# Optimization experiments

Hardware: AMD Instinct MI355X
Metric: run time of the kernel (lower is better)

The kernel has to match this reference:

```python
import jax, jax.numpy as jnp
import numpy as np

DIM = 1024
HEADS = 16
HEAD_DIM = DIM // HEADS
SCALE = HEAD_DIM ** -0.5
EPS = 1e-5


def _ln(x, g, b):
    m = jnp.mean(x, axis=-1, keepdims=True)
    v = jnp.mean((x - m) ** 2, axis=-1, keepdims=True)
    return (x - m) * jax.lax.rsqrt(v + EPS) * g + b


def setup_inputs() -> dict:
    key = jax.random.key(0)
    ks = jax.random.split(key, 12)
    B, N, C = 4, 1024, DIM
    s = lambda fan: 1.0 / np.sqrt(fan)
    return {
        "src_q": jax.random.normal(ks[0], (B, N, C), jnp.float32),
        "src_kv": jax.random.normal(ks[1], (B, N, C), jnp.float32),
        "gq": jnp.ones((C,), jnp.float32), "bq": jnp.zeros((C,), jnp.float32),
        "gkv": jnp.ones((C,), jnp.float32), "bkv": jnp.zeros((C,), jnp.float32),
        "Wq": jax.random.normal(ks[2], (C, C), jnp.float32) * s(C),
        "Wkv": jax.random.normal(ks[3], (C, 2 * C), jnp.float32) * s(C),
        "Wproj": jax.random.normal(ks[4], (C, C), jnp.float32) * s(C),
        "bproj": jnp.zeros((C,), jnp.float32),
        "gn": jnp.ones((C,), jnp.float32), "bn": jnp.zeros((C,), jnp.float32),
        "W1": jax.random.normal(ks[5], (C, 4 * C), jnp.float32) * s(C),
        "b1": jnp.zeros((4 * C,), jnp.float32),
        "W2": jax.random.normal(ks[6], (4 * C, C), jnp.float32) * s(4 * C),
        "b2": jnp.zeros((C,), jnp.float32),
    }


def reference(src_q, src_kv, gq, bq, gkv, bkv, Wq, Wkv, Wproj, bproj,
              gn, bn, W1, b1, W2, b2):
    B, N, C = src_q.shape
    qn = _ln(src_q, gq, bq)
    kvn = _ln(src_kv, gkv, bkv)
    # Q: [B, H, N, d]
    Q = (qn @ Wq).reshape(B, N, HEADS, HEAD_DIM).transpose(0, 2, 1, 3)
    KV = (kvn @ Wkv).reshape(B, N, 2, HEADS, HEAD_DIM).transpose(2, 0, 3, 1, 4)
    K, V = KV[0], KV[1]
    attn = jnp.einsum('bhqd,bhkd->bhqk', Q, K) * SCALE
    attn = jax.nn.softmax(attn, axis=-1)
    # NOTE: original code multiplies by scale a second time here (faithful)
    x = jnp.einsum('bhqk,bhkd->bhqd', attn, V) * SCALE
    x = x.transpose(0, 2, 1, 3).reshape(B, N, C)
    x = x @ Wproj + bproj
    src = src_q + x               # residual (drop_path = identity in eval)
    src = _ln(src, gn, bn)
    h = jax.nn.gelu(src @ W1 + b1, approximate=False)
    src2 = h @ W2 + b2
    return src + src2
```

## Files before the change

### kernel.cpp

```cpp
#include <hip/hip_runtime.h>
#include <hip/hip_bf16.h>
#include <math.h>

typedef __bf16 bf16;
typedef __bf16 bf16x2 __attribute__((ext_vector_type(2)));
typedef __bf16 bf16x8 __attribute__((ext_vector_type(8)));
typedef float f32x4 __attribute__((ext_vector_type(4)));
typedef float f32x16 __attribute__((ext_vector_type(16)));
typedef unsigned int u32;
typedef unsigned int u32x2 __attribute__((ext_vector_type(2)));
typedef unsigned int u32x4 __attribute__((ext_vector_type(4)));

#define SCALE 0.125f
#define L2E 1.4426950408889634f

#define GLOAD_LDS16(gptr, lptr)                                      \
  __builtin_amdgcn_global_load_lds(                                  \
      (const __attribute__((address_space(1))) void*)(gptr),         \
      (__attribute__((address_space(3))) void*)(lptr), 16, 0, 0)

__device__ __forceinline__ u32 pk_bf16(float lo, float hi) {
  bf16x2 t;
  t[0] = (bf16)lo;
  t[1] = (bf16)hi;
  return __builtin_bit_cast(u32, t);
}

__device__ __forceinline__ void plane32_swap(u32& a, u32& b) {
  asm volatile("v_permlane32_swap_b32 %0, %1" : "+v"(a), "+v"(b));
}

__global__ __launch_bounds__(256) void ln_f32(const float* __restrict__ x,
                                              const float* __restrict__ g,
                                              const float* __restrict__ b,
                                              bf16* __restrict__ y) {
  long base = (long)blockIdx.x * 1024;
  int tid = threadIdx.x;
  float v[4];
#pragma unroll
  for (int i = 0; i < 4; i++) v[i] = x[base + tid + i * 256];
  float s1 = v[0] + v[1] + v[2] + v[3];
  float s2 = v[0] * v[0] + v[1] * v[1] + v[2] * v[2] + v[3] * v[3];
#pragma unroll
  for (int off = 32; off; off >>= 1) {
    s1 += __shfl_xor(s1, off);
    s2 += __shfl_xor(s2, off);
  }
  __shared__ float aux[2][4];
  int wave = tid >> 6, lane = tid & 63;
  if (lane == 0) { aux[0][wave] = s1; aux[1][wave] = s2; }
  __syncthreads();
  float S1 = aux[0][0] + aux[0][1] + aux[0][2] + aux[0][3];
  float S2 = aux[1][0] + aux[1][1] + aux[1][2] + aux[1][3];
  float mean = S1 * (1.0f / 1024.0f);
  float var = S2 * (1.0f / 1024.0f) - mean * mean;
  float rs = rsqrtf(var + 1e-5f);
#pragma unroll
  for (int i = 0; i < 4; i++) {
    int c = tid + i * 256;
    y[base + c] = (bf16)(((v[i] - mean) * rs) * g[c] + b[c]);
  }
}

__global__ __launch_bounds__(256) void transpose_w(const float* __restrict__ W,
                                                   bf16* __restrict__ Wt,
                                                   int K, int N) {
  __shared__ bf16 tile[64][66];
  int n0 = blockIdx.x * 64, k0 = blockIdx.y * 64;
  int c = threadIdx.x & 63, r4 = threadIdx.x >> 6;
#pragma unroll
  for (int i = 0; i < 16; i++)
    tile[i * 4 + r4][c] = (bf16)W[(long)(k0 + i * 4 + r4) * N + n0 + c];
  __syncthreads();
#pragma unroll
  for (int i = 0; i < 16; i++)
    Wt[(long)(n0 + i * 4 + r4) * K + k0 + c] = tile[c][i * 4 + r4];
}

__global__ __launch_bounds__(256) void extract_vt(const bf16* __restrict__ KV,
                                                  bf16* __restrict__ Vt) {
  __shared__ bf16 tile[64][66];
  int bh = blockIdx.z, b = bh >> 4, h = bh & 15;
  const bf16* src = KV + (long)b * 1024 * 2048 + 1024 + h * 64;
  bf16* dst = Vt + (long)bh * 64 * 1024;
  int n0 = blockIdx.x * 64;
  int c = threadIdx.x & 63, r4 = threadIdx.x >> 6;
#pragma unroll
  for (int i = 0; i < 16; i++)
    tile[i * 4 + r4][c] = src[(long)(n0 + i * 4 + r4) * 2048 + c];
  __syncthreads();
#pragma unroll
  for (int i = 0; i < 16; i++)
    dst[(long)(i * 4 + r4) * 1024 + n0 + c] = tile[c][i * 4 + r4];
}

__global__ __launch_bounds__(256) void attn_fused(
    const bf16* __restrict__ Q,
    const bf16* __restrict__ KV,
    const bf16* __restrict__ Vt,
    bf16* __restrict__ X) {
  __shared__ __align__(16) bf16 Qs[128 * 64];
  __shared__ __align__(16) bf16 Ks[2][64 * 128];
  __shared__ __align__(16) bf16 Vs[2][64 * 128];
  int tid = threadIdx.x, wave = tid >> 6, lane = tid & 63;
  int l31 = lane & 31, h = lane >> 5;
  int bh = blockIdx.y, b = bh >> 4, hd = bh & 15;
  const bf16* Qb = Q + (long)b * 1048576 + hd * 64;
  const bf16* Kb = KV + (long)b * 2097152 + hd * 64;
  const bf16* Vb = Vt + (long)bh * 65536;
  bf16* Xb = X + (long)b * 1048576 + hd * 64;
  int q0 = blockIdx.x * 128;

  const bf16* gk[4];
  const bf16* gv[4];
  int eoKV[4];
#pragma unroll
  for (int t = 0; t < 4; t++) {
    int eo = (t * 256 + tid) * 8;
    eoKV[t] = eo;
    int r2 = eo >> 7, pp = (eo & 127) >> 3, q = pp ^ (r2 & 15);
    gk[t] = &Kb[(long)(r2 + ((q >> 3) << 6)) * 2048 + ((q & 7) << 3)];
    gv[t] = &Vb[(long)r2 * 1024 + (q << 3)];
  }

#pragma unroll
  for (int t = 0; t < 4; t++) {
    int eo = (t * 256 + tid) * 8;
    int r = eo >> 6, p = (eo & 63) >> 3;
    int c = (p ^ (r & 7)) << 3;
    GLOAD_LDS16(&Qb[(long)(q0 + r) * 1024 + c], &Qs[eo]);
  }
#pragma unroll
  for (int t = 0; t < 4; t++) GLOAD_LDS16(gk[t], &Ks[0][eoKV[t]]);
#pragma unroll
  for (int t = 0; t < 4; t++) GLOAD_LDS16(gv[t], &Vs[0][eoKV[t]]);
  __syncthreads();

  bf16x8 qf[4];
  {
    int r = wave * 32 + l31;
#pragma unroll
    for (int dw = 0; dw < 4; dw++) {
      int p = (dw * 2 + h) ^ (r & 7);
      qf[dw] = *(const bf16x8*)&Qs[r * 64 + p * 8];
    }
  }

  const float C = 0.18033688011112042f;
  float m_run = -1e30f, l_run = 0.0f;
  f32x16 acc[2] = {};
  int cur = 0;

  for (int kc = 0; kc < 8; kc++) {
    if (kc < 7) {
#pragma unroll
      for (int t = 0; t < 4; t++)
        GLOAD_LDS16(gk[t] + (long)(kc + 1) * 128 * 2048, &Ks[cur ^ 1][eoKV[t]]);
#pragma unroll
      for (int t = 0; t < 4; t++)
        GLOAD_LDS16(gv[t] + (kc + 1) * 128, &Vs[cur ^ 1][eoKV[t]]);
    }
    const bf16* ks = Ks[cur];
    const bf16* vs = Vs[cur];

    f32x16 s[4] = {};
#pragma unroll
    for (int kt = 0; kt < 4; kt++) {
      int k = kt * 32 + l31;
      int r2 = k & 63, hi = k >> 6;
#pragma unroll
      for (int dw = 0; dw < 4; dw++) {
        int p = (hi * 8 + dw * 2 + h) ^ (r2 & 15);
        bf16x8 kf = *(const bf16x8*)&ks[r2 * 128 + p * 8];
        s[kt] = __builtin_amdgcn_mfma_f32_32x32x16_bf16(kf, qf[dw], s[kt], 0, 0, 0);
      }
    }

    float mk[4];
#pragma unroll
    for (int kt = 0; kt < 4; kt++) {
      float m01 = fmaxf(fmaxf(s[kt][0], s[kt][1]), fmaxf(s[kt][2], s[kt][3]));
      float m23 = fmaxf(fmaxf(s[kt][4], s[kt][5]), fmaxf(s[kt][6], s[kt][7]));
      float m45 = fmaxf(fmaxf(s[kt][8], s[kt][9]), fmaxf(s[kt][10], s[kt][11]));
      float m67 = fmaxf(fmaxf(s[kt][12], s[kt][13]), fmaxf(s[kt][14], s[kt][15]));
      mk[kt] = fmaxf(fmaxf(m01, m23), fmaxf(m45, m67));
    }
    float mx = fmaxf(fmaxf(mk[0], mk[1]), fmaxf(mk[2], mk[3]));
    mx = fmaxf(mx, __shfl_xor(mx, 32));
    float m_new = fmaxf(m_run, mx);
    float alpha = exp2f((m_run - m_new) * C);
    m_run = m_new;
    float mc = m_new * C;
    float rk[4];
#pragma unroll
    for (int kt = 0; kt < 4; kt++) {
      float r0 = 0.0f;
#pragma unroll
      for (int r = 0; r < 16; r++) {
        float pv = exp2f(s[kt][r] * C - mc);
        s[kt][r] = pv;
        r0 += pv;
      }
      rk[kt] = r0;
    }
    float rs = (rk[0] + rk[1]) + (rk[2] + rk[3]);
    rs += __shfl_xor(rs, 32);
    l_run = l_run * alpha + rs;
#pragma unroll
    for (int nt = 0; nt < 2; nt++)
#pragma unroll
      for (int r = 0; r < 16; r++) acc[nt][r] *= alpha;

#pragma unroll
    for (int kw = 0; kw < 8; kw++) {
      int kt = kw >> 1, rb = (kw & 1) * 8;
      u32 wA = pk_bf16(s[kt][rb + 0], s[kt][rb + 1]);
      u32 wB = pk_bf16(s[kt][rb + 2], s[kt][rb + 3]);
      u32 wC = pk_bf16(s[kt][rb + 4], s[kt][rb + 5]);
      u32 wD = pk_bf16(s[kt][rb + 6], s[kt][rb + 7]);
      plane32_swap(wA, wC);
      plane32_swap(wB, wD);
      u32x4 wv = {wA, wB, wC, wD};
      bf16x8 pf = __builtin_bit_cast(bf16x8, wv);
#pragma unroll
      for (int nt = 0; nt < 2; nt++) {
        int r2 = nt * 32 + l31;
        int p = (kw * 2 + h) ^ (r2 & 15);
        bf16x8 vf = *(const bf16x8*)&vs[r2 * 128 + p * 8];
        acc[nt] = __builtin_amdgcn_mfma_f32_32x32x16_bf16(vf, pf, acc[nt], 0, 0, 0);
      }
    }

    if (kc < 7) {
      __syncthreads();
      cur ^= 1;
    }
  }

  float fs = SCALE / l_run;
  bf16* Os = Qs;
  int qrow = wave * 32 + l31;
#pragma unroll
  for (int nt = 0; nt < 2; nt++)
#pragma unroll
    for (int g = 0; g < 4; g++) {
      u32 w0 = pk_bf16(acc[nt][g * 4 + 0] * fs, acc[nt][g * 4 + 1] * fs);
      u32 w1 = pk_bf16(acc[nt][g * 4 + 2] * fs, acc[nt][g * 4 + 3] * fs);
      int s8 = nt * 8 + g * 2 + h;
      int phys = s8 ^ (qrow & 15);
      u32x2 wv = {w0, w1};
      *(u32x2*)&Os[qrow * 64 + phys * 4] = wv;
    }
  int rrow = wave * 32 + (lane >> 1);
  int cbase = (lane & 1) * 32;
#pragma unroll
  for (int t2 = 0; t2 < 4; t2++) {
    int s0 = (lane & 1) * 8 + t2 * 2;
    u32x2 a = *(u32x2*)&Os[rrow * 64 + ((s0 ^ (rrow & 15)) * 4)];
    u32x2 bb = *(u32x2*)&Os[rrow * 64 + (((s0 + 1) ^ (rrow & 15)) * 4)];
    u32x4 o4 = {a[0], a[1], bb[0], bb[1]};
    *(u32x4*)&Xb[(long)(q0 + rrow) * 1024 + cbase + t2 * 8] = o4;
  }
}

template <int BM, int BN, int BK, int WR, int WC, int EPI, int CF32, int RBF16>
__global__ __launch_bounds__(256) void gemm_t(
    const bf16* __restrict__ A, long sA_lo, long sA_hi, int lda,
    const bf16* __restrict__ B, long sB_lo, long sB_hi, int ldb,
    void* __restrict__ Cv, long sC_lo, long sC_hi, int ldc,
    int K,
    const float* __restrict__ bias,
    const void* __restrict__ resv, int ldr) {
  constexpr int MT = BM / (16 * WR);
  constexpr int NT = BN / (16 * WC);
  constexpr int KS = BK / 32;
  constexpr int ACH = BM * BK / 2048;
  constexpr int BCH = BN * BK / 2048;
  __shared__ __align__(16) bf16 As[BM * BK];
  __shared__ __align__(16) bf16 Bs[BN * BK];
  int tid = threadIdx.x;
  int wave = tid >> 6, lane = tid & 63;
  int wm = wave / WC, wn = wave % WC;
  int quad = lane >> 4, l16 = lane & 15;
  int zhi = blockIdx.z >> 4, zlo = blockIdx.z & 15;
  const bf16* Ab = A + zhi * sA_hi + zlo * sA_lo;
  const bf16* Bb = B + zhi * sB_hi + zlo * sB_lo;
  long coff = zhi * sC_hi + zlo * sC_lo;
  int m0 = blockIdx.y * BM, n0 = blockIdx.x * BN;

  f32x4 acc[MT][NT] = {};

  for (int kt = 0; kt < K; kt += BK) {
    __syncthreads();
#pragma unroll
    for (int t = 0; t < ACH; t++) {
      int eo = (t * 256 + tid) * 8;
      int r = eo / BK, p = (eo % BK) >> 3;
      int c = (p ^ (r & 7)) << 3;
      GLOAD_LDS16(&Ab[(long)(m0 + r) * lda + kt + c], &As[eo]);
    }
#pragma unroll
    for (int t = 0; t < BCH; t++) {
      int eo = (t * 256 + tid) * 8;
      int r = eo / BK, p = (eo % BK) >> 3;
      int c = (p ^ (r & 7)) << 3;
      GLOAD_LDS16(&Bb[(long)(n0 + r) * ldb + kt + c], &Bs[eo]);
    }
    __syncthreads();
    bf16x8 af[KS][MT], bfr[KS][NT];
#pragma unroll
    for (int ks = 0; ks < KS; ks++) {
#pragma unroll
      for (int mt = 0; mt < MT; mt++) {
        int row = wm * MT * 16 + mt * 16 + l16;
        int p = (ks * 4 + quad) ^ (row & 7);
        af[ks][mt] = *(const bf16x8*)&As[row * BK + p * 8];
      }
#pragma unroll
      for (int nt = 0; nt < NT; nt++) {
        int row = wn * NT * 16 + nt * 16 + l16;
        int p = (ks * 4 + quad) ^ (row & 7);
        bfr[ks][nt] = *(const bf16x8*)&Bs[row * BK + p * 8];
      }
    }
#pragma unroll
    for (int ks = 0; ks < KS; ks++)
#pragma unroll
      for (int mt = 0; mt < MT; mt++)
#pragma unroll
        for (int nt = 0; nt < NT; nt++)
          acc[mt][nt] = __builtin_amdgcn_mfma_f32_16x16x32_bf16(
              af[ks][mt], bfr[ks][nt], acc[mt][nt], 0, 0, 0);
  }

  int gm = m0 + wm * MT * 16, gn = n0 + wn * NT * 16;
#pragma unroll
  for (int nt = 0; nt < NT; nt++) {
    int col = gn + nt * 16 + l16;
    float bv = (EPI != 0) ? bias[col] : 0.0f;
#pragma unroll
    for (int mt = 0; mt < MT; mt++) {
#pragma unroll
      for (int r = 0; r < 4; r++) {
        int row = gm + mt * 16 + quad * 4 + r;
        float v = acc[mt][nt][r] + bv;
        if (EPI == 2) {
          v = 0.5f * v * (1.0f + erff(v * 0.70710678118654752f));
        } else if (EPI == 1) {
          float rv = RBF16 ? (float)((const bf16*)resv)[(long)row * ldr + col]
                           : ((const float*)resv)[(long)row * ldr + col];
          v += rv;
        }
        if (CF32)
          ((float*)Cv)[coff + (long)row * ldc + col] = v;
        else
          ((bf16*)Cv)[coff + (long)row * ldc + col] = (bf16)v;
      }
    }
  }
}

extern "C" void kernel_launch(void* const* d_in, const int* in_sizes, int n_in,
                              void* d_out, int out_size, void* d_ws, size_t ws_size,
                              hipStream_t stream) {
  const float* src_q  = (const float*)d_in[0];
  const float* src_kv = (const float*)d_in[1];
  const float* gq     = (const float*)d_in[2];
  const float* bq     = (const float*)d_in[3];
  const float* gkv    = (const float*)d_in[4];
  const float* bkv    = (const float*)d_in[5];
  const float* Wq     = (const float*)d_in[6];
  const float* Wkv    = (const float*)d_in[7];
  const float* Wproj  = (const float*)d_in[8];
  const float* bproj  = (const float*)d_in[9];
  const float* gn     = (const float*)d_in[10];
  const float* bn     = (const float*)d_in[11];
  const float* W1     = (const float*)d_in[12];
  const float* b1     = (const float*)d_in[13];
  const float* W2     = (const float*)d_in[14];
  const float* b2     = (const float*)d_in[15];
  float* out = (float*)d_out;

  char* ws = (char*)d_ws;
  const long MB = 1024 * 1024;
  bf16* Wq_t    = (bf16*)(ws + 0 * MB);
  bf16* Wkv_t   = (bf16*)(ws + 2 * MB);
  bf16* Wproj_t = (bf16*)(ws + 6 * MB);
  bf16* W1_t    = (bf16*)(ws + 8 * MB);
  bf16* W2_t    = (bf16*)(ws + 16 * MB);
  bf16* qn      = (bf16*)(ws + 24 * MB);
  bf16* kvn     = (bf16*)(ws + 32 * MB);
  bf16* Qm      = (bf16*)(ws + 40 * MB);
  bf16* KVm     = (bf16*)(ws + 48 * MB);
  bf16* Vt      = (bf16*)(ws + 64 * MB);
  bf16* xbuf    = (bf16*)(ws + 24 * MB);
  float* tbuf   = (float*)(ws + 48 * MB);
  bf16* sbuf    = (bf16*)(ws + 64 * MB);
  bf16* hbuf    = (bf16*)(ws + 72 * MB);

  transpose_w<<<dim3(16, 16), 256, 0, stream>>>(Wq, Wq_t, 1024, 1024);
  transpose_w<<<dim3(32, 16), 256, 0, stream>>>(Wkv, Wkv_t, 1024, 2048);
  transpose_w<<<dim3(16, 16), 256, 0, stream>>>(Wproj, Wproj_t, 1024, 1024);
  transpose_w<<<dim3(64, 16), 256, 0, stream>>>(W1, W1_t, 1024, 4096);
  transpose_w<<<dim3(16, 64), 256, 0, stream>>>(W2, W2_t, 4096, 1024);

  ln_f32<<<4096, 256, 0, stream>>>(src_q, gq, bq, qn);
  ln_f32<<<4096, 256, 0, stream>>>(src_kv, gkv, bkv, kvn);

  gemm_t<128, 64, 64, 4, 1, 0, 0, 0><<<dim3(16, 32, 1), 256, 0, stream>>>(
      qn, 0, 0, 1024, Wq_t, 0, 0, 1024, Qm, 0, 0, 1024, 1024,
      nullptr, nullptr, 0);
  gemm_t<128, 128, 64, 2, 2, 0, 0, 0><<<dim3(16, 32, 1), 256, 0, stream>>>(
      kvn, 0, 0, 1024, Wkv_t, 0, 0, 1024, KVm, 0, 0, 2048, 1024,
      nullptr, nullptr, 0);
  extract_vt<<<dim3(16, 1, 64), 256, 0, stream>>>(KVm, Vt);

  attn_fused<<<dim3(8, 64), 256, 0, stream>>>(Qm, KVm, Vt, xbuf);

  gemm_t<128, 64, 64, 4, 1, 1, 1, 0><<<dim3(16, 32, 1), 256, 0, stream>>>(
      xbuf, 0, 0, 1024, Wproj_t, 0, 0, 1024, tbuf, 0, 0, 1024, 1024,
      bproj, src_q, 1024);
  ln_f32<<<4096, 256, 0, stream>>>(tbuf, gn, bn, sbuf);
  gemm_t<128, 128, 64, 2, 2, 2, 0, 0><<<dim3(32, 32, 1), 256, 0, stream>>>(
      sbuf, 0, 0, 1024, W1_t, 0, 0, 1024, hbuf, 0, 0, 4096, 1024,
      b1, nullptr, 0);
  gemm_t<128, 64, 64, 4, 1, 1, 1, 1><<<dim3(16, 32, 1), 256, 0, stream>>>(
      hbuf, 0, 0, 4096, W2_t, 0, 0, 4096, out, 0, 0, 1024, 4096,
      b2, sbuf, 1024);
}
```

Baseline: 405.4 us.

## Replace GEMM with triple-buffered 512-thread pipelined kernel and larger tiles

Replaces the single-buffered gemm_t with gemm_p, which uses three LDS stages and prefetches two K-tiles ahead through direct global-to-LDS loads. Waits use explicit vmcnt counters, and the loop issues its barriers, setprio and sched_barrier calls manually, so that loads overlap the MFMA work. Blocks grow to 512 threads with 128x128 or 256x128 tiles, which cuts the number of workgroups and raises reuse of each loaded tile. The cost is more LDS per block (up to about 144KB) and fewer blocks, which can lower occupancy and leave the grid short of a full wave on some GEMMs.

New measurement: 372.0 us. -8.3%, faster.

```diff
diff --git a/kernel.cpp b/kernel.cpp
--- a/kernel.cpp
+++ b/kernel.cpp
@@ -12,12 +12,19 @@
 typedef unsigned int u32x4 __attribute__((ext_vector_type(4)));
 
 #define SCALE 0.125f
-#define L2E 1.4426950408889634f
 
 #define GLOAD_LDS16(gptr, lptr)                                      \
   __builtin_amdgcn_global_load_lds(                                  \
       (const __attribute__((address_space(1))) void*)(gptr),         \
       (__attribute__((address_space(3))) void*)(lptr), 16, 0, 0)
+
+template <int N>
+__device__ __forceinline__ void vmcnt_wait() {
+  if constexpr (N == 0) asm volatile("s_waitcnt vmcnt(0)" ::: "memory");
+  else if constexpr (N == 4) asm volatile("s_waitcnt vmcnt(4)" ::: "memory");
+  else if constexpr (N == 6) asm volatile("s_waitcnt vmcnt(6)" ::: "memory");
+  else static_assert(N == 0 || N == 4 || N == 6, "unsupported vmcnt");
+}
 
 __device__ __forceinline__ u32 pk_bf16(float lo, float hi) {
   bf16x2 t;
@@ -263,87 +270,127 @@
   }
 }
 
-template <int BM, int BN, int BK, int WR, int WC, int EPI, int CF32, int RBF16>
-__global__ __launch_bounds__(256) void gemm_t(
-    const bf16* __restrict__ A, long sA_lo, long sA_hi, int lda,
-    const bf16* __restrict__ B, long sB_lo, long sB_hi, int ldb,
-    void* __restrict__ Cv, long sC_lo, long sC_hi, int ldc,
-    int K,
+template <int BM, int BN, int WR, int WC, int PH, int EPI, int CF32, int RBF16>
+__global__ __launch_bounds__(512) void gemm_p(
+    const bf16* __restrict__ A, int lda,
+    const bf16* __restrict__ B, int ldb,
+    void* __restrict__ Cv, int ldc, int K,
     const float* __restrict__ bias,
     const void* __restrict__ resv, int ldr) {
   constexpr int MT = BM / (16 * WR);
   constexpr int NT = BN / (16 * WC);
-  constexpr int KS = BK / 32;
-  constexpr int ACH = BM * BK / 2048;
-  constexpr int BCH = BN * BK / 2048;
-  __shared__ __align__(16) bf16 As[BM * BK];
-  __shared__ __align__(16) bf16 Bs[BN * BK];
+  constexpr int KSP = 2 / PH;
+  constexpr int L = (BM + BN) / 64;
+  constexpr int LA = BM / 64;
+  constexpr int AE = BM * 64;
+  constexpr int BUFE = (BM + BN) * 64;
+  __shared__ __align__(16) bf16 lds[3 * BUFE];
   int tid = threadIdx.x;
   int wave = tid >> 6, lane = tid & 63;
   int wm = wave / WC, wn = wave % WC;
   int quad = lane >> 4, l16 = lane & 15;
-  int zhi = blockIdx.z >> 4, zlo = blockIdx.z & 15;
-  const bf16* Ab = A + zhi * sA_hi + zlo * sA_lo;
-  const bf16* Bb = B + zhi * sB_hi + zlo * sB_lo;
-  long coff = zhi * sC_hi + zlo * sC_lo;
   int m0 = blockIdx.y * BM, n0 = blockIdx.x * BN;
 
+  const bf16* gp[L];
+  int lo[L];
+#pragma unroll
+  for (int i = 0; i < L; i++) {
+    if (i < LA) {
+      int eo = (i * 512 + tid) * 8;
+      int r = eo >> 6, p = (eo & 63) >> 3;
+      int c = (p ^ (r & 7)) << 3;
+      gp[i] = &A[(long)(m0 + r) * lda + c];
+      lo[i] = eo;
+    } else {
+      int eo = ((i - LA) * 512 + tid) * 8;
+      int r = eo >> 6, p = (eo & 63) >> 3;
+      int c = (p ^ (r & 7)) << 3;
+      gp[i] = &B[(long)(n0 + r) * ldb + c];
+      lo[i] = AE + eo;
+    }
+  }
+
+  int ntk = K >> 6;
+#pragma unroll
+  for (int i = 0; i < L; i++) GLOAD_LDS16(gp[i], &lds[lo[i]]);
+#pragma unroll
+  for (int i = 0; i < L; i++) gp[i] += 64;
+#pragma unroll
+  for (int i = 0; i < L; i++) GLOAD_LDS16(gp[i], &lds[BUFE + lo[i]]);
+#pragma unroll
+  for (int i = 0; i < L; i++) gp[i] += 64;
+  vmcnt_wait<L>();
+  asm volatile("" ::: "memory");
+  __builtin_amdgcn_s_barrier();
+
   f32x4 acc[MT][NT] = {};
-
-  for (int kt = 0; kt < K; kt += BK) {
-    __syncthreads();
-#pragma unroll
-    for (int t = 0; t < ACH; t++) {
-      int eo = (t * 256 + tid) * 8;
-      int r = eo / BK, p = (eo % BK) >> 3;
-      int c = (p ^ (r & 7)) << 3;
-      GLOAD_LDS16(&Ab[(long)(m0 + r) * lda + kt + c], &As[eo]);
-    }
-#pragma unroll
-    for (int t = 0; t < BCH; t++) {
-      int eo = (t * 256 + tid) * 8;
-      int r = eo / BK, p = (eo % BK) >> 3;
-      int c = (p ^ (r & 7)) << 3;
-      GLOAD_LDS16(&Bb[(long)(n0 + r) * ldb + kt + c], &Bs[eo]);
-    }
-    __syncthreads();
-    bf16x8 af[KS][MT], bfr[KS][NT];
-#pragma unroll
-    for (int ks = 0; ks < KS; ks++) {
-#pragma unroll
-      for (int mt = 0; mt < MT; mt++) {
-        int row = wm * MT * 16 + mt * 16 + l16;
-        int p = (ks * 4 + quad) ^ (row & 7);
-        af[ks][mt] = *(const bf16x8*)&As[row * BK + p * 8];
-      }
-#pragma unroll
-      for (int nt = 0; nt < NT; nt++) {
-        int row = wn * NT * 16 + nt * 16 + l16;
-        int p = (ks * 4 + quad) ^ (row & 7);
-        bfr[ks][nt] = *(const bf16x8*)&Bs[row * BK + p * 8];
-      }
-    }
-#pragma unroll
-    for (int ks = 0; ks < KS; ks++)
-#pragma unroll
-      for (int mt = 0; mt < MT; mt++)
-#pragma unroll
-        for (int nt = 0; nt < NT; nt++)
-          acc[mt][nt] = __builtin_amdgcn_mfma_f32_16x16x32_bf16(
-              af[ks][mt], bfr[ks][nt], acc[mt][nt], 0, 0, 0);
-  }
-
-  int gm = m0 + wm * MT * 16, gn = n0 + wn * NT * 16;
+  int b = 0;
+  for (int t = 0; t < ntk; t++) {
+    const bf16* Al = &lds[b * BUFE];
+    const bf16* Bl = &lds[b * BUFE + AE];
+    int b2 = b + 2; if (b2 >= 3) b2 -= 3;
+    bool more = (t + 2) < ntk;
+#pragma unroll
+    for (int ph = 0; ph < PH; ph++) {
+      bf16x8 af[KSP][MT], bv[KSP][NT];
+#pragma unroll
+      for (int k2 = 0; k2 < KSP; k2++) {
+        int ks = ph * KSP + k2;
+#pragma unroll
+        for (int mt = 0; mt < MT; mt++) {
+          int row = wm * (BM / WR) + mt * 16 + l16;
+          int p = (ks * 4 + quad) ^ (row & 7);
+          af[k2][mt] = *(const bf16x8*)&Al[row * 64 + p * 8];
+        }
+#pragma unroll
+        for (int nt = 0; nt < NT; nt++) {
+          int row = wn * (BN / WC) + nt * 16 + l16;
+          int p = (ks * 4 + quad) ^ (row & 7);
+          bv[k2][nt] = *(const bf16x8*)&Bl[row * 64 + p * 8];
+        }
+      }
+      if (more) {
+#pragma unroll
+        for (int i = ph * L / PH; i < (ph + 1) * L / PH; i++)
+          GLOAD_LDS16(gp[i], &lds[b2 * BUFE + lo[i]]);
+      }
+      if (ph == PH - 1) {
+        if (more) vmcnt_wait<L>();
+        else vmcnt_wait<0>();
+      }
+      asm volatile("" ::: "memory");
+      __builtin_amdgcn_s_barrier();
+      asm volatile("s_waitcnt lgkmcnt(0)" ::: "memory");
+      __builtin_amdgcn_sched_barrier(0);
+      __builtin_amdgcn_s_setprio(1);
+#pragma unroll
+      for (int k2 = 0; k2 < KSP; k2++)
+#pragma unroll
+        for (int mt = 0; mt < MT; mt++)
+#pragma unroll
+          for (int nt = 0; nt < NT; nt++)
+            acc[mt][nt] = __builtin_amdgcn_mfma_f32_16x16x32_bf16(
+                af[k2][mt], bv[k2][nt], acc[mt][nt], 0, 0, 0);
+      __builtin_amdgcn_s_setprio(0);
+      __builtin_amdgcn_sched_barrier(0);
+      __builtin_amdgcn_s_barrier();
+    }
+#pragma unroll
+    for (int i = 0; i < L; i++) gp[i] += 64;
+    b += 1; if (b == 3) b = 0;
+  }
+
+  int gm = m0 + wm * (BM / WR), gn = n0 + wn * (BN / WC);
 #pragma unroll
   for (int nt = 0; nt < NT; nt++) {
     int col = gn + nt * 16 + l16;
-    float bv = (EPI != 0) ? bias[col] : 0.0f;
+    float bvb = (EPI != 0) ? bias[col] : 0.0f;
 #pragma unroll
     for (int mt = 0; mt < MT; mt++) {
 #pragma unroll
       for (int r = 0; r < 4; r++) {
         int row = gm + mt * 16 + quad * 4 + r;
-        float v = acc[mt][nt][r] + bv;
+        float v = acc[mt][nt][r] + bvb;
         if (EPI == 2) {
           v = 0.5f * v * (1.0f + erff(v * 0.70710678118654752f));
         } else if (EPI == 1) {
@@ -352,9 +399,9 @@
           v += rv;
         }
         if (CF32)
-          ((float*)Cv)[coff + (long)row * ldc + col] = v;
+          ((float*)Cv)[(long)row * ldc + col] = v;
         else
-          ((bf16*)Cv)[coff + (long)row * ldc + col] = (bf16)v;
+          ((bf16*)Cv)[(long)row * ldc + col] = (bf16)v;
       }
     }
   }
@@ -407,24 +454,19 @@
   ln_f32<<<4096, 256, 0, stream>>>(src_q, gq, bq, qn);
   ln_f32<<<4096, 256, 0, stream>>>(src_kv, gkv, bkv, kvn);
 
-  gemm_t<128, 64, 64, 4, 1, 0, 0, 0><<<dim3(16, 32, 1), 256, 0, stream>>>(
-      qn, 0, 0, 1024, Wq_t, 0, 0, 1024, Qm, 0, 0, 1024, 1024,
-      nullptr, nullptr, 0);
-  gemm_t<128, 128, 64, 2, 2, 0, 0, 0><<<dim3(16, 32, 1), 256, 0, stream>>>(
-      kvn, 0, 0, 1024, Wkv_t, 0, 0, 1024, KVm, 0, 0, 2048, 1024,
-      nullptr, nullptr, 0);
+  gemm_p<128, 128, 2, 4, 1, 0, 0, 0><<<dim3(8, 32), 512, 0, stream>>>(
+      qn, 1024, Wq_t, 1024, Qm, 1024, 1024, nullptr, nullptr, 0);
+  gemm_p<256, 128, 4, 2, 2, 0, 0, 0><<<dim3(16, 16), 512, 0, stream>>>(
+      kvn, 1024, Wkv_t, 1024, KVm, 2048, 1024, nullptr, nullptr, 0);
   extract_vt<<<dim3(16, 1, 64), 256, 0, stream>>>(KVm, Vt);
 
   attn_fused<<<dim3(8, 64), 256, 0, stream>>>(Qm, KVm, Vt, xbuf);
 
-  gemm_t<128, 64, 64, 4, 1, 1, 1, 0><<<dim3(16, 32, 1), 256, 0, stream>>>(
-      xbuf, 0, 0, 1024, Wproj_t, 0, 0, 1024, tbuf, 0, 0, 1024, 1024,
-      bproj, src_q, 1024);
+  gemm_p<128, 128, 2, 4, 1, 1, 1, 0><<<dim3(8, 32), 512, 0, stream>>>(
+      xbuf, 1024, Wproj_t, 1024, tbuf, 1024, 1024, bproj, src_q, 1024);
   ln_f32<<<4096, 256, 0, stream>>>(tbuf, gn, bn, sbuf);
-  gemm_t<128, 128, 64, 2, 2, 2, 0, 0><<<dim3(32, 32, 1), 256, 0, stream>>>(
-      sbuf, 0, 0, 1024, W1_t, 0, 0, 1024, hbuf, 0, 0, 4096, 1024,
-      b1, nullptr, 0);
-  gemm_t<128, 64, 64, 4, 1, 1, 1, 1><<<dim3(16, 32, 1), 256, 0, stream>>>(
-      hbuf, 0, 0, 4096, W2_t, 0, 0, 4096, out, 0, 0, 1024, 4096,
-      b2, sbuf, 1024);
-}
+  gemm_p<256, 128, 4, 2, 2, 2, 0, 0><<<dim3(32, 16), 512, 0, stream>>>(
+      sbuf, 1024, W1_t, 1024, hbuf, 4096, 1024, b1, nullptr, 0);
+  gemm_p<128, 128, 2, 4, 1, 1, 1, 1><<<dim3(8, 32), 512, 0, stream>>>(
+      hbuf, 4096, W2_t, 4096, out, 1024, 4096, b2, sbuf, 1024);
+}
```
